# Kernel tuning notes

Measured on AMD Instinct MI355X. Metric: run time of the kernel, lower is better.

## Reference

```python
import jax, jax.numpy as jnp
import numpy as np

B, T, VOCAB = 8192, 1024, 10000

def setup_inputs() -> dict:
    key = jax.random.key(0)
    k1, k2, k3, k4 = jax.random.split(key, 4)
    sample_seq = jax.random.randint(k1, (B, T), 0, VOCAB, dtype=jnp.int32)
    sample_seqLogprobs = jax.random.normal(k2, (B, T), dtype=jnp.float32)
    sample_value = jax.random.normal(k3, (B, T), dtype=jnp.float32)
    sample_reward = jax.random.normal(k4, (B, T), dtype=jnp.float32)
    return {
        "sample_seq": sample_seq,
        "sample_seqLogprobs": sample_seqLogprobs,
        "sample_value": sample_value,
        "sample_reward": sample_reward,
    }

def reference(sample_seq, sample_seqLogprobs, sample_value, sample_reward):
    # Vectorized version of the per-element python loop: zero out every token
    # at or after the first EOS (token id 0). cumsum>0 of the EOS indicator is
    # the running-max (cummax) of (seq==0).
    at_or_after_eos = jnp.cumsum((sample_seq == 0).astype(jnp.int32), axis=1) > 0
    seq = jnp.where(at_or_after_eos, 0, sample_seq)  # [B, T]

    # mask = (seq>0), shifted right by one with a leading column of ones
    mask = (seq > 0).astype(sample_seqLogprobs.dtype)
    mask = jnp.concatenate(
        [jnp.ones((mask.shape[0], 1), mask.dtype), mask[:, :-1]], axis=1
    )

    # sample_reward is a detached numpy array in the original (no grad)
    reward = jax.lax.stop_gradient(sample_reward)
    reward_diff = reward - sample_value  # [B, T]

    # masked REINFORCE loss, normalized by number of valid tokens
    output = -sample_seqLogprobs * reward_diff * mask
    loss = output.sum() / mask.sum()
    return loss
```

## Files before the change

### kernel.cpp

```cpp
#include <hip/hip_runtime.h>

#define BROWS 8192
#define TLEN  1024
#define NBLK  2048
#define RPB   4

__global__ __launch_bounds__(256) void fz_kernel(
    const int* __restrict__ seq,
    int*       __restrict__ fz_out)
{
    const int row  = blockIdx.x * 4 + (threadIdx.x >> 6);
    const int lane = threadIdx.x & 63;

    const int4* s4 = (const int4*)(seq + (size_t)row * TLEN);
    int4 s[4];
    #pragma unroll
    for (int k = 0; k < 4; ++k)
        s[k] = s4[k * 64 + lane];

    int fz = TLEN;
    #pragma unroll
    for (int k = 3; k >= 0; --k) {
        const int base = k * 256 + lane * 4;
        if (s[k].w == 0) fz = base + 3;
        if (s[k].z == 0) fz = base + 2;
        if (s[k].y == 0) fz = base + 1;
        if (s[k].x == 0) fz = base + 0;
    }
    #pragma unroll
    for (int off = 32; off > 0; off >>= 1)
        fz = min(fz, __shfl_xor(fz, off, 64));

    if (lane == 0) fz_out[row] = fz;
}

__global__ __launch_bounds__(256) void sum_kernel(
    const float* __restrict__ logp,
    const float* __restrict__ value,
    const float* __restrict__ reward,
    const int*   __restrict__ fz_in,
    double*      __restrict__ blk_sum)
{
    const int tid = threadIdx.x;

    float4 l[RPB], v[RPB], r[RPB];
    int    fz[RPB];
    #pragma unroll
    for (int k = 0; k < RPB; ++k) {
        const int    row = blockIdx.x + k * NBLK;
        const size_t off = (size_t)row * TLEN;
        l[k]  = ((const float4*)(logp   + off))[tid];
        v[k]  = ((const float4*)(value  + off))[tid];
        r[k]  = ((const float4*)(reward + off))[tid];
        fz[k] = fz_in[row];
    }

    const int t0 = tid * 4;
    double acc = 0.0;
    #pragma unroll
    for (int k = 0; k < RPB; ++k) {
        if (t0 + 0 <= fz[k]) acc += (double)(-l[k].x * (r[k].x - v[k].x));
        if (t0 + 1 <= fz[k]) acc += (double)(-l[k].y * (r[k].y - v[k].y));
        if (t0 + 2 <= fz[k]) acc += (double)(-l[k].z * (r[k].z - v[k].z));
        if (t0 + 3 <= fz[k]) acc += (double)(-l[k].w * (r[k].w - v[k].w));
    }

    #pragma unroll
    for (int off = 32; off > 0; off >>= 1)
        acc += __shfl_xor(acc, off, 64);

    __shared__ double ls[4];
    if ((tid & 63) == 0) ls[tid >> 6] = acc;
    __syncthreads();
    if (tid == 0)
        blk_sum[blockIdx.x] = ls[0] + ls[1] + ls[2] + ls[3];
}

__global__ __launch_bounds__(256) void final_kernel(
    const double* __restrict__ blk_sum,
    const int*    __restrict__ fz_in,
    float*        __restrict__ out)
{
    const int tid  = threadIdx.x;
    const int lane = tid & 63;
    const int wave = tid >> 6;

    double s = 0.0, c = 0.0;
    for (int i = tid; i < NBLK; i += 256)
        s += blk_sum[i];
    for (int i = tid; i < BROWS; i += 256)
        c += (double)min(fz_in[i] + 1, TLEN);

    #pragma unroll
    for (int off = 32; off > 0; off >>= 1) {
        s += __shfl_xor(s, off, 64);
        c += __shfl_xor(c, off, 64);
    }
    __shared__ double ls[4], lc[4];
    if (lane == 0) { ls[wave] = s; lc[wave] = c; }
    __syncthreads();
    if (tid == 0) {
        double ts = ls[0] + ls[1] + ls[2] + ls[3];
        double tc = lc[0] + lc[1] + lc[2] + lc[3];
        out[0] = (float)(ts / tc);
    }
}

extern "C" void kernel_launch(void* const* d_in, const int* in_sizes, int n_in,
                              void* d_out, int out_size, void* d_ws, size_t ws_size,
                              hipStream_t stream) {
    const int*   seq    = (const int*)  d_in[0];
    const float* logp   = (const float*)d_in[1];
    const float* value  = (const float*)d_in[2];
    const float* reward = (const float*)d_in[3];
    float* out = (float*)d_out;

    int*    fz      = (int*)d_ws;
    double* blk_sum = (double*)((char*)d_ws + 65536);

    fz_kernel   <<<BROWS / 4, 256, 0, stream>>>(seq, fz);
    sum_kernel  <<<NBLK,      256, 0, stream>>>(logp, value, reward, fz, blk_sum);
    final_kernel<<<1,         256, 0, stream>>>(blk_sum, fz, out);
}
```

Baseline: 156.0 us.

## Fuse final reduction into sum kernel via atomics and last-block completion

Removes the separate final reduction kernel. Per-row valid-token counts are now accumulated with a double atomicAdd in the EOS-scan kernel, and the sum kernel adds its block partial atomically, with the last arriving block computing the ratio. Both kernels now use persistent-style grids that loop over multiple rows per wave or block. This trades one kernel launch and a serial tail for a memset plus global atomics, and makes the floating-point summation order nondeterministic.

```diff
diff --git a/kernel.cpp b/kernel.cpp
--- a/kernel.cpp
+++ b/kernel.cpp
@@ -2,36 +2,50 @@
 
 #define BROWS 8192
 #define TLEN  1024
-#define NBLK  2048
-#define RPB   4
+#define GRID_A 512
+#define GRID_B 1024
+#define ITER_B (BROWS / GRID_B)
+
 
 __global__ __launch_bounds__(256) void fz_kernel(
     const int* __restrict__ seq,
-    int*       __restrict__ fz_out)
+    int*       __restrict__ fz_out,
+    double*    __restrict__ cnt_acc)
 {
-    const int row  = blockIdx.x * 4 + (threadIdx.x >> 6);
+    const int wave = threadIdx.x >> 6;
     const int lane = threadIdx.x & 63;
+    const int wid  = blockIdx.x * 4 + wave;
 
-    const int4* s4 = (const int4*)(seq + (size_t)row * TLEN);
-    int4 s[4];
+    double c = 0.0;
     #pragma unroll
-    for (int k = 0; k < 4; ++k)
-        s[k] = s4[k * 64 + lane];
+    for (int it = 0; it < 4; ++it) {
+        const int row = wid + it * 2048;
+        const int4* s4 = (const int4*)(seq + (size_t)row * TLEN);
+        int4 s[4];
+        #pragma unroll
+        for (int k = 0; k < 4; ++k)
+            s[k] = s4[k * 64 + lane];
 
-    int fz = TLEN;
-    #pragma unroll
-    for (int k = 3; k >= 0; --k) {
-        const int base = k * 256 + lane * 4;
-        if (s[k].w == 0) fz = base + 3;
-        if (s[k].z == 0) fz = base + 2;
-        if (s[k].y == 0) fz = base + 1;
-        if (s[k].x == 0) fz = base + 0;
+        int fz = TLEN;
+        #pragma unroll
+        for (int k = 3; k >= 0; --k) {
+            const int base = k * 256 + lane * 4;
+            if (s[k].w == 0) fz = base + 3;
+            if (s[k].z == 0) fz = base + 2;
+            if (s[k].y == 0) fz = base + 1;
+            if (s[k].x == 0) fz = base + 0;
+        }
+        #pragma unroll
+        for (int off = 32; off > 0; off >>= 1)
+            fz = min(fz, __shfl_xor(fz, off, 64));
+
+        if (lane == 0) {
+            fz_out[row] = fz;
+            c += (double)min(fz + 1, TLEN);
+        }
     }
-    #pragma unroll
-    for (int off = 32; off > 0; off >>= 1)
-        fz = min(fz, __shfl_xor(fz, off, 64));
-
-    if (lane == 0) fz_out[row] = fz;
+    if (lane == 0)
+        atomicAdd(cnt_acc, c);
 }
 
 __global__ __launch_bounds__(256) void sum_kernel(
@@ -39,70 +53,45 @@
     const float* __restrict__ value,
     const float* __restrict__ reward,
     const int*   __restrict__ fz_in,
-    double*      __restrict__ blk_sum)
+    double*      __restrict__ sum_acc,
+    double*      __restrict__ cnt_acc,
+    int*         __restrict__ arrive,
+    float*       __restrict__ out)
 {
     const int tid = threadIdx.x;
+    const int t0  = tid * 4;
 
-    float4 l[RPB], v[RPB], r[RPB];
-    int    fz[RPB];
-    #pragma unroll
-    for (int k = 0; k < RPB; ++k) {
-        const int    row = blockIdx.x + k * NBLK;
+    double acc = 0.0;
+    #pragma unroll 2
+    for (int it = 0; it < ITER_B; ++it) {
+        const int row = blockIdx.x + it * GRID_B;
+        const int fz  = fz_in[row];
         const size_t off = (size_t)row * TLEN;
-        l[k]  = ((const float4*)(logp   + off))[tid];
-        v[k]  = ((const float4*)(value  + off))[tid];
-        r[k]  = ((const float4*)(reward + off))[tid];
-        fz[k] = fz_in[row];
-    }
-
-    const int t0 = tid * 4;
-    double acc = 0.0;
-    #pragma unroll
-    for (int k = 0; k < RPB; ++k) {
-        if (t0 + 0 <= fz[k]) acc += (double)(-l[k].x * (r[k].x - v[k].x));
-        if (t0 + 1 <= fz[k]) acc += (double)(-l[k].y * (r[k].y - v[k].y));
-        if (t0 + 2 <= fz[k]) acc += (double)(-l[k].z * (r[k].z - v[k].z));
-        if (t0 + 3 <= fz[k]) acc += (double)(-l[k].w * (r[k].w - v[k].w));
+        const float4 l = ((const float4*)(logp   + off))[tid];
+        const float4 v = ((const float4*)(value  + off))[tid];
+        const float4 r = ((const float4*)(reward + off))[tid];
+        if (t0 + 0 <= fz) acc += (double)(-l.x * (r.x - v.x));
+        if (t0 + 1 <= fz) acc += (double)(-l.y * (r.y - v.y));
+        if (t0 + 2 <= fz) acc += (double)(-l.z * (r.z - v.z));
+        if (t0 + 3 <= fz) acc += (double)(-l.w * (r.w - v.w));
     }
 
     #pragma unroll
     for (int off = 32; off > 0; off >>= 1)
         acc += __shfl_xor(acc, off, 64);
-
     __shared__ double ls[4];
     if ((tid & 63) == 0) ls[tid >> 6] = acc;
     __syncthreads();
-    if (tid == 0)
-        blk_sum[blockIdx.x] = ls[0] + ls[1] + ls[2] + ls[3];
-}
 
-__global__ __launch_bounds__(256) void final_kernel(
-    const double* __restrict__ blk_sum,
-    const int*    __restrict__ fz_in,
-    float*        __restrict__ out)
-{
-    const int tid  = threadIdx.x;
-    const int lane = tid & 63;
-    const int wave = tid >> 6;
-
-    double s = 0.0, c = 0.0;
-    for (int i = tid; i < NBLK; i += 256)
-        s += blk_sum[i];
-    for (int i = tid; i < BROWS; i += 256)
-        c += (double)min(fz_in[i] + 1, TLEN);
-
-    #pragma unroll
-    for (int off = 32; off > 0; off >>= 1) {
-        s += __shfl_xor(s, off, 64);
-        c += __shfl_xor(c, off, 64);
-    }
-    __shared__ double ls[4], lc[4];
-    if (lane == 0) { ls[wave] = s; lc[wave] = c; }
-    __syncthreads();
     if (tid == 0) {
-        double ts = ls[0] + ls[1] + ls[2] + ls[3];
-        double tc = lc[0] + lc[1] + lc[2] + lc[3];
-        out[0] = (float)(ts / tc);
+        atomicAdd(sum_acc, ls[0] + ls[1] + ls[2] + ls[3]);
+        __threadfence();
+        const int old = atomicAdd(arrive, 1);
+        if (old == GRID_B - 1) {
+            const double s = atomicAdd(sum_acc, 0.0);
+            const double c = atomicAdd(cnt_acc, 0.0);
+            out[0] = (float)(s / c);
+        }
     }
 }
 
@@ -115,10 +104,14 @@
     const float* reward = (const float*)d_in[3];
     float* out = (float*)d_out;
 
-    int*    fz      = (int*)d_ws;
-    double* blk_sum = (double*)((char*)d_ws + 65536);
+    double* sum_acc = (double*)d_ws;
+    double* cnt_acc = sum_acc + 1;
+    int*    arrive  = (int*)((char*)d_ws + 16);
+    int*    fz      = (int*)((char*)d_ws + 64);
 
-    fz_kernel   <<<BROWS / 4, 256, 0, stream>>>(seq, fz);
-    sum_kernel  <<<NBLK,      256, 0, stream>>>(logp, value, reward, fz, blk_sum);
-    final_kernel<<<1,         256, 0, stream>>>(blk_sum, fz, out);
+    hipMemsetAsync(d_ws, 0, 24, stream);
+
+    fz_kernel <<<GRID_A, 256, 0, stream>>>(seq, fz, cnt_acc);
+    sum_kernel<<<GRID_B, 256, 0, stream>>>(logp, value, reward, fz,
+                                           sum_acc, cnt_acc, arrive, out);
 }
```

Result: slower. 220.3 us (+41.3%).
